# Optimization experiments

Hardware: AMD Instinct MI355X
Metric: run time of the kernel (lower is better)

The kernel has to match this reference:

```python
import jax, jax.numpy as jnp
import numpy as np

B, S, D, H = 2, 2048, 2048, 16
HD = D // H          # head_dim = 128
FF = 8192            # intermediate_size
LN_EPS = 1e-05
BIT_EPS = 1e-05


def _rope_tables(seq_len, head_dim):
    inv_freq = 1.0 / (10000.0 ** (np.arange(0, head_dim, 2, dtype=np.float64) / head_dim))
    ang = np.arange(seq_len, dtype=np.float64)[:, None] * inv_freq[None, :]  # [S, HD/2]
    ang = np.concatenate([ang, ang], axis=-1)  # [S, HD]
    return jnp.asarray(np.cos(ang), jnp.float32), jnp.asarray(np.sin(ang), jnp.float32)


def setup_inputs() -> dict:
    key = jax.random.key(0)
    ks = jax.random.split(key, 9)
    hidden_states = jax.random.normal(ks[0], (B, S, D), jnp.float32)
    # causal additive mask [1, S, S]
    causal = jnp.tril(jnp.ones((S, S), bool))
    attention_mask = jnp.where(causal, 0.0, -1e9)[None].astype(jnp.float32)
    cos, sin = _rope_tables(S, HD)
    w = lambda k, o, i: jax.random.normal(k, (o, i), jnp.float32) * 0.02
    return {
        'hidden_states': hidden_states,
        'attention_mask': attention_mask,
        'cos': cos, 'sin': sin,
        'wq': w(ks[1], D, D), 'wk': w(ks[2], D, D),
        'wv': w(ks[3], D, D), 'wo': w(ks[4], D, D),
        'wg': w(ks[5], FF, D), 'wu': w(ks[6], FF, D), 'wd': w(ks[7], D, FF),
        'ln1_w': jnp.ones((D,), jnp.float32),
        'ln2_w': jnp.ones((D,), jnp.float32),
    }


def bitlinear(x, w):
    # ternarize: clamp(round(w / (mean|w| + eps)), -1, 1); int8 cast in torch
    # breaks grad through the ternary values -> stop_gradient here.
    scale = jnp.mean(jnp.abs(w))
    tern = jax.lax.stop_gradient(jnp.clip(jnp.round(w / (scale + BIT_EPS)), -1.0, 1.0))
    # dequant = ternary * mean|w|, then standard linear (x @ W^T)
    return jnp.einsum('bsi,oi->bso', x, tern * scale)


def rmsnorm(x, w, eps=LN_EPS):
    var = jnp.mean(jnp.square(x.astype(jnp.float32)), axis=-1, keepdims=True)
    return w * (x * jax.lax.rsqrt(var + eps))


def rotate_half(x):
    x1, x2 = jnp.split(x, 2, axis=-1)
    return jnp.concatenate([-x2, x1], axis=-1)


def apply_rope(q, k, cos, sin):
    # q, k: [B, S, D] -> per-head rope -> back to [B, S, D]
    qh = q.reshape(B, S, H, HD)
    kh = k.reshape(B, S, H, HD)
    c = cos[None, :, None, :]
    s = sin[None, :, None, :]
    qe = qh * c + rotate_half(qh) * s
    ke = kh * c + rotate_half(kh) * s
    return qe.reshape(B, S, D), ke.reshape(B, S, D)


def reference(hidden_states, attention_mask, cos, sin,
              wq, wk, wv, wo, wg, wu, wd, ln1_w, ln2_w):
    residual = hidden_states
    # --- attention block ---
    x = rmsnorm(hidden_states, ln1_w)
    q = bitlinear(x, wq)
    k = bitlinear(x, wk)
    v = bitlinear(x, wv)
    q, k = apply_rope(q, k, cos, sin)
    # NOTE: scores over FULL hidden dim (no head split), scaled by sqrt(head_dim),
    # exactly as in the original module.
    scores = jnp.einsum('bsd,btd->bst', q, k) / jnp.sqrt(jnp.float32(HD))
    scores = scores + attention_mask
    probs = jax.nn.softmax(scores, axis=-1)
    attn_out = jnp.einsum('bst,btd->bsd', probs, v)
    attn_out = bitlinear(attn_out, wo)
    h = residual + attn_out
    # --- MLP block ---
    residual = h
    y = rmsnorm(h, ln2_w)
    gated = bitlinear(y, wg) * bitlinear(y, wu)
    out = bitlinear(gated, wd)
    return residual + out
```

## Files before the change

kernel.cpp:

```cpp
#include <hip/hip_runtime.h>
#include <stdint.h>

#define DEV __device__ __forceinline__

typedef __attribute__((ext_vector_type(8))) short short8;
typedef __attribute__((ext_vector_type(8))) __bf16 bf16x8;
typedef __attribute__((ext_vector_type(4))) float f32x4;

DEV unsigned short f2bf(float f) {
  union { float f; unsigned int u; } v; v.f = f;
  unsigned int r = v.u + 0x7fffu + ((v.u >> 16) & 1u);
  return (unsigned short)(r >> 16);
}
DEV float bf2f(unsigned short h) {
  union { unsigned int u; float f; } v; v.u = ((unsigned int)h) << 16;
  return v.f;
}
DEV f32x4 mfma16(short8 a, short8 b, f32x4 c) {
  return __builtin_amdgcn_mfma_f32_16x16x32_bf16(
      __builtin_bit_cast(bf16x8, a), __builtin_bit_cast(bf16x8, b), c, 0, 0, 0);
}
DEV void gload_lds16(const void* g, void* lds) {
  __builtin_amdgcn_global_load_lds(
      (const __attribute__((address_space(1))) void*)g,
      (__attribute__((address_space(3))) void*)lds, 16, 0, 0);
}

struct MArgs {
  const float* src[7];
  unsigned short* dst[7];
  int n[7];
  int sidx[7];
};

__global__ __launch_bounds__(256) void absmean_partial_multi(
    MArgs a, float* __restrict__ partial) {
  const int m = blockIdx.y;
  const float4* w4 = (const float4*)a.src[m];
  const int n4 = a.n[m] >> 2;
  float s = 0.f;
  for (int i = blockIdx.x * 256 + threadIdx.x; i < n4; i += 1024 * 256) {
    float4 v = w4[i];
    s += fabsf(v.x) + fabsf(v.y) + fabsf(v.z) + fabsf(v.w);
  }
#pragma unroll
  for (int mm = 1; mm < 64; mm <<= 1) s += __shfl_xor(s, mm);
  __shared__ float red[4];
  if ((threadIdx.x & 63) == 0) red[threadIdx.x >> 6] = s;
  __syncthreads();
  if (threadIdx.x == 0)
    partial[m * 1024 + blockIdx.x] = red[0] + red[1] + red[2] + red[3];
}

__global__ __launch_bounds__(256) void absmean_final(
    const float* __restrict__ partial, float* __restrict__ scales) {
  __shared__ double red[256];
  const int m = blockIdx.x;
  double s = 0.0;
  for (int i = threadIdx.x; i < 1024; i += 256) s += (double)partial[m * 1024 + i];
  red[threadIdx.x] = s;
  __syncthreads();
  for (int t = 128; t > 0; t >>= 1) {
    if (threadIdx.x < t) red[threadIdx.x] += red[threadIdx.x + t];
    __syncthreads();
  }
  if (threadIdx.x == 0) {
    const long long cnt = (m < 4) ? 4194304ll : 16777216ll;
    scales[m] = (float)(red[0] / (double)cnt);
  }
}

__global__ __launch_bounds__(256) void quantize_multi(
    MArgs a, const float* __restrict__ scales) {
  const int m = blockIdx.y;
  const float sc = scales[a.sidx[m]];
  const float inv = 1.f / (sc + 1e-5f);
  const float4* src = (const float4*)a.src[m];
  ushort4* dst = (ushort4*)a.dst[m];
  const int n4 = a.n[m] >> 2;
  for (int i = blockIdx.x * 256 + threadIdx.x; i < n4; i += 2048 * 256) {
    float4 v = src[i];
    ushort4 o;
    o.x = f2bf(fminf(fmaxf(rintf(v.x * inv), -1.f), 1.f) * sc);
    o.y = f2bf(fminf(fmaxf(rintf(v.y * inv), -1.f), 1.f) * sc);
    o.z = f2bf(fminf(fmaxf(rintf(v.z * inv), -1.f), 1.f) * sc);
    o.w = f2bf(fminf(fmaxf(rintf(v.w * inv), -1.f), 1.f) * sc);
    dst[i] = o;
  }
}

__global__ __launch_bounds__(256) void rmsnorm_k(
    const float* __restrict__ x, const float* __restrict__ wt,
    unsigned short* __restrict__ out) {
  const long long t = blockIdx.x;
  const float* xr = x + t * 2048;
  const int i0 = threadIdx.x * 8;
  float4 a = *(const float4*)(xr + i0);
  float4 b = *(const float4*)(xr + i0 + 4);
  float ss = a.x * a.x + a.y * a.y + a.z * a.z + a.w * a.w +
             b.x * b.x + b.y * b.y + b.z * b.z + b.w * b.w;
#pragma unroll
  for (int m = 1; m < 64; m <<= 1) ss += __shfl_xor(ss, m);
  __shared__ float red[4];
  if ((threadIdx.x & 63) == 0) red[threadIdx.x >> 6] = ss;
  __syncthreads();
  float tot = red[0] + red[1] + red[2] + red[3];
  float rs = rsqrtf(tot * (1.f / 2048.f) + 1e-5f);
  float4 wa = *(const float4*)(wt + i0);
  float4 wb = *(const float4*)(wt + i0 + 4);
  ushort4 o1, o2;
  o1.x = f2bf(a.x * wa.x * rs); o1.y = f2bf(a.y * wa.y * rs);
  o1.z = f2bf(a.z * wa.z * rs); o1.w = f2bf(a.w * wa.w * rs);
  o2.x = f2bf(b.x * wb.x * rs); o2.y = f2bf(b.y * wb.y * rs);
  o2.z = f2bf(b.z * wb.z * rs); o2.w = f2bf(b.w * wb.w * rs);
  *(ushort4*)(out + t * 2048 + i0) = o1;
  *(ushort4*)(out + t * 2048 + i0 + 4) = o2;
}

__global__ __launch_bounds__(256) void combine_rms(
    const float* __restrict__ ep, const float* __restrict__ p,
    const float* __restrict__ wt, float* __restrict__ hout,
    unsigned short* __restrict__ yout) {
  const long long t = blockIdx.x;
  const int i0 = threadIdx.x * 8;
  const long long base = t * 2048 + i0;
  float4 e1 = *(const float4*)(ep + base);
  float4 e2 = *(const float4*)(ep + base + 4);
  float4 p1 = *(const float4*)(p + base);
  float4 p2 = *(const float4*)(p + base + 4);
  float4 q1 = *(const float4*)(p + 8388608 + base);
  float4 q2 = *(const float4*)(p + 8388608 + base + 4);
  float h[8] = {e1.x + p1.x + q1.x, e1.y + p1.y + q1.y,
                e1.z + p1.z + q1.z, e1.w + p1.w + q1.w,
                e2.x + p2.x + q2.x, e2.y + p2.y + q2.y,
                e2.z + p2.z + q2.z, e2.w + p2.w + q2.w};
  float4 h1 = {h[0], h[1], h[2], h[3]};
  float4 h2 = {h[4], h[5], h[6], h[7]};
  *(float4*)(hout + base) = h1;
  *(float4*)(hout + base + 4) = h2;
  float ss = 0.f;
#pragma unroll
  for (int i = 0; i < 8; ++i) ss += h[i] * h[i];
#pragma unroll
  for (int m = 1; m < 64; m <<= 1) ss += __shfl_xor(ss, m);
  __shared__ float red[4];
  if ((threadIdx.x & 63) == 0) red[threadIdx.x >> 6] = ss;
  __syncthreads();
  const float tot = red[0] + red[1] + red[2] + red[3];
  const float rs = rsqrtf(tot * (1.f / 2048.f) + 1e-5f);
  float4 wa = *(const float4*)(wt + i0);
  float4 wb = *(const float4*)(wt + i0 + 4);
  ushort4 o1, o2;
  o1.x = f2bf(h[0] * wa.x * rs); o1.y = f2bf(h[1] * wa.y * rs);
  o1.z = f2bf(h[2] * wa.z * rs); o1.w = f2bf(h[3] * wa.w * rs);
  o2.x = f2bf(h[4] * wb.x * rs); o2.y = f2bf(h[5] * wb.y * rs);
  o2.z = f2bf(h[6] * wb.z * rs); o2.w = f2bf(h[7] * wb.w * rs);
  *(ushort4*)(yout + base) = o1;
  *(ushort4*)(yout + base + 4) = o2;
}

__global__ __launch_bounds__(256) void rope_k(
    const unsigned short* __restrict__ qkv, const float* __restrict__ cosT,
    const float* __restrict__ sinT, unsigned short* __restrict__ qr,
    unsigned short* __restrict__ kr, unsigned short* __restrict__ vt) {
  const long long gid = (long long)blockIdx.x * 256 + threadIdx.x;
  const int t = (int)(gid >> 10);
  const int r = (int)(gid & 1023);
  const int h = r >> 6, d = r & 63;
  const int s = t & 2047, b = t >> 11;
  const unsigned short* row = qkv + (long long)t * 6144;
  const float c = cosT[s * 128 + d], sn = sinT[s * 128 + d];
  const int col = h * 128 + d;
  const float SC = 0.08838834764831845f;
  float q1 = bf2f(row[col]), q2 = bf2f(row[col + 64]);
  float k1 = bf2f(row[2048 + col]), k2 = bf2f(row[2048 + col + 64]);
  long long ob = (long long)t * 2048 + col;
  qr[ob] = f2bf((q1 * c - q2 * sn) * SC);
  qr[ob + 64] = f2bf((q2 * c + q1 * sn) * SC);
  kr[ob] = f2bf(k1 * c - k2 * sn);
  kr[ob + 64] = f2bf(k2 * c + k1 * sn);
  vt[((long long)b * 2048 + col) * 2048 + s] = row[4096 + col];
  vt[((long long)b * 2048 + col + 64) * 2048 + s] = row[4096 + col + 64];
}

__global__ __launch_bounds__(256) void softmax_causal(
    const float* __restrict__ scores, unsigned short* __restrict__ probs) {
  const int r = blockIdx.x;
  const int s = r & 2047;
  const float* src = scores + (long long)r * 2048;
  unsigned short* dst = probs + (long long)r * 2048;
  const int L = s + 1;
  const int j0 = threadIdx.x * 8;
  float4 a = *(const float4*)(src + j0);
  float4 b = *(const float4*)(src + j0 + 4);
  float v[8] = {a.x, a.y, a.z, a.w, b.x, b.y, b.z, b.w};
  float mx = -1e30f;
#pragma unroll
  for (int i = 0; i < 8; ++i) {
    if (j0 + i >= L) v[i] = -1e30f;
    mx = fmaxf(mx, v[i]);
  }
#pragma unroll
  for (int m = 1; m < 64; m <<= 1) mx = fmaxf(mx, __shfl_xor(mx, m));
  __shared__ float redM[4], redS[4];
  if ((threadIdx.x & 63) == 0) redM[threadIdx.x >> 6] = mx;
  __syncthreads();
  mx = fmaxf(fmaxf(redM[0], redM[1]), fmaxf(redM[2], redM[3]));
  float sum = 0.f;
#pragma unroll
  for (int i = 0; i < 8; ++i) {
    v[i] = (j0 + i < L) ? __expf(v[i] - mx) : 0.f;
    sum += v[i];
  }
#pragma unroll
  for (int m = 1; m < 64; m <<= 1) sum += __shfl_xor(sum, m);
  if ((threadIdx.x & 63) == 0) redS[threadIdx.x >> 6] = sum;
  __syncthreads();
  const float inv = 1.f / (redS[0] + redS[1] + redS[2] + redS[3]);
  ushort4 o1, o2;
  o1.x = f2bf(v[0] * inv); o1.y = f2bf(v[1] * inv);
  o1.z = f2bf(v[2] * inv); o1.w = f2bf(v[3] * inv);
  o2.x = f2bf(v[4] * inv); o2.y = f2bf(v[5] * inv);
  o2.z = f2bf(v[6] * inv); o2.w = f2bf(v[7] * inv);
  *(ushort4*)(dst + j0) = o1;
  *(ushort4*)(dst + j0 + 4) = o2;
}

template <int EPI, int CAUSAL>
__global__ __launch_bounds__(512, 2) void gemm256(
    const unsigned short* __restrict__ A, const unsigned short* __restrict__ Bw,
    void* __restrict__ Cp, const void* __restrict__ Ep,
    int N, int K, int nbx, int kLen, int ngTot,
    long long sAz, long long sBz, long long zCout) {
  __shared__ __align__(16) unsigned short lds[4 * 2 * 8192];
  __shared__ __align__(16) unsigned short ldsDummy[512];
  const int tid = threadIdx.x;
  const int wid = tid >> 6, l = tid & 63;
  const int wr = wid >> 2, wcn = wid & 3;

  const int nwg = gridDim.x;
  const int q8 = nwg >> 3;
  const int lin = (blockIdx.x & 7) * q8 + (blockIdx.x >> 3);
  const int t32 = lin >> 5, r32 = lin & 31;
  const int tpr = nbx >> 3;
  const int tm = t32 / tpr, tn = t32 - tm * tpr;
  const long long m0 = (long long)(tm * 4 + (r32 >> 3)) * 256;
  const long long n0 = (long long)(tn * 8 + (r32 & 7)) * 256;
  if (CAUSAL == 1 && n0 > m0) return;
  const int z = blockIdx.z;
  A += z * sAz;
  Bw += z * sBz;
  const long long kbase = (long long)z * kLen;
  const long long zofs = (long long)z * zCout;
  int ng = ngTot;
  if (CAUSAL == 2) {
    const int lim = (int)((m0 + 256) >> 5);
    ng = lim < ng ? lim : ng;
  }

  const int stRow = (l >> 2);
  const int stCol = (((l & 3) ^ ((l >> 3) & 3))) * 8;
  auto stage = [&](int chunk, int sslot) {
    if (chunk < ng) {
      char* base = (char*)lds + (sslot * 2) * 16384;
      const long long kcol = kbase + (long long)chunk * 32 + stCol;
#pragma unroll
      for (int i = 0; i < 2; ++i) {
        const int row = (wid * 2 + i) * 16 + stRow;
        gload_lds16(&A[(m0 + row) * K + kcol], base + (wid * 2 + i) * 1024);
        gload_lds16(&Bw[(n0 + row) * K + kcol],
                    base + 16384 + (wid * 2 + i) * 1024);
      }
    } else {
#pragma unroll
      for (int i = 0; i < 4; ++i) gload_lds16(&A[m0 * K], (char*)ldsDummy);
    }
  };

  const int ar = l & 15;
  const int rj = ((l >> 4) ^ ((l >> 1) & 3)) << 4;
  const int aoff = (wr * 128 + ar) * 64 + rj;
  const int boff = (wcn * 64 + ar) * 64 + rj;

  f32x4 acc[8][4] = {};
  short8 aX[4], bX[4], aY[4], bY[4];

  stage(0, 0); stage(1, 1); stage(2, 2);
  asm volatile("s_waitcnt vmcnt(4)" ::: "memory");
  __builtin_amdgcn_s_barrier();
#pragma unroll
  for (int m = 0; m < 4; ++m)
    aX[m] = *(const short8*)((const char*)lds + aoff + m * 1024);
#pragma unroll
  for (int n = 0; n < 4; ++n)
    bX[n] = *(const short8*)((const char*)lds + 16384 + boff + n * 1024);

#define CHUNK_BODY(SLOT, NSLOT, SYNC, cur03, curB, nxt03, nxtB, cc)            \
  {                                                                            \
    const char* sAc = (const char*)lds + (SLOT * 2) * 16384;                   \
    const char* sAn = (const char*)lds + (NSLOT * 2) * 16384;                  \
    const char* sBn = (const char*)lds + (NSLOT * 2 + 1) * 16384;              \
    short8 a47[4];                                                             \
    _Pragma("unroll") for (int m = 0; m < 4; ++m)                              \
        a47[m] = *(const short8*)(sAc + aoff + 4096 + m * 1024);               \
    stage((cc) + 3, (SLOT + 3) & 3);                                           \
    __builtin_amdgcn_s_setprio(1);                                             \
    _Pragma("unroll") for (int m = 0; m < 4; ++m)                              \
      _Pragma("unroll") for (int n = 0; n < 4; ++n)                            \
          acc[m][n] = mfma16(cur03[m], curB[n], acc[m][n]);                    \
    __builtin_amdgcn_s_setprio(0);                                             \
    if (SYNC) {                                                                \
      asm volatile("s_waitcnt vmcnt(4)" ::: "memory");                         \
      __builtin_amdgcn_s_barrier();                                            \
    }                                                                          \
    _Pragma("unroll") for (int m = 0; m < 4; ++m)                              \
        nxt03[m] = *(const short8*)(sAn + aoff + m * 1024);                    \
    _Pragma("unroll") for (int n = 0; n < 4; ++n)                              \
        nxtB[n] = *(const short8*)(sBn + boff + n * 1024);                     \
    __builtin_amdgcn_s_setprio(1);                                             \
    _Pragma("unroll") for (int m = 0; m < 4; ++m)                              \
      _Pragma("unroll") for (int n = 0; n < 4; ++n)                            \
          acc[m + 4][n] = mfma16(a47[m], curB[n], acc[m + 4][n]);              \
    __builtin_amdgcn_s_setprio(0);                                             \
  }

  for (int c = 0; c < ng; c += 4) {
    CHUNK_BODY(0, 1, false, aX, bX, aY, bY, c);
    CHUNK_BODY(1, 2, true, aY, bY, aX, bX, c + 1);
    CHUNK_BODY(2, 3, false, aX, bX, aY, bY, c + 2);
    CHUNK_BODY(3, 0, true, aY, bY, aX, bX, c + 3);
  }
#undef CHUNK_BODY
  asm volatile("s_waitcnt vmcnt(0)" ::: "memory");
  __builtin_amdgcn_s_barrier();

  const int orow = (l >> 4) * 4, ocol = l & 15;
#pragma unroll
  for (int m = 0; m < 8; ++m)
#pragma unroll
    for (int n = 0; n < 4; ++n)
#pragma unroll
      for (int r = 0; r < 4; ++r) {
        const long long gr = m0 + wr * 128 + m * 16 + orow + r;
        const long long gc = n0 + wcn * 64 + n * 16 + ocol;
        const long long idx = zofs + gr * N + gc;
        const float v = acc[m][n][r];
        if (EPI == 0) {
          ((unsigned short*)Cp)[idx] = f2bf(v);
        } else if (EPI == 2) {
          ((unsigned short*)Cp)[idx] = f2bf(bf2f(((const unsigned short*)Ep)[idx]) * v);
        } else {
          ((float*)Cp)[idx] = v;
        }
      }
}

__global__ __launch_bounds__(256) void combine2(
    const float* __restrict__ ep, const float* __restrict__ p,
    float* __restrict__ out, long long n4) {
  const float4* e4 = (const float4*)ep;
  const float4* p4 = (const float4*)p;
  float4* o4 = (float4*)out;
  for (long long i = blockIdx.x * 256 + threadIdx.x; i < n4; i += 2048 * 256) {
    float4 a = e4[i], b = p4[i], c = p4[i + n4];
    float4 o;
    o.x = a.x + b.x + c.x; o.y = a.y + b.y + c.y;
    o.z = a.z + b.z + c.z; o.w = a.w + b.w + c.w;
    o4[i] = o;
  }
}

extern "C" void kernel_launch(void* const* d_in, const int* in_sizes, int n_in,
                              void* d_out, int out_size, void* d_ws, size_t ws_size,
                              hipStream_t stream) {
  (void)in_sizes; (void)n_in; (void)out_size; (void)ws_size;
  const float* hidden = (const float*)d_in[0];
  const float* cosT = (const float*)d_in[2];
  const float* sinT = (const float*)d_in[3];
  const float* wq = (const float*)d_in[4];
  const float* wk = (const float*)d_in[5];
  const float* wv = (const float*)d_in[6];
  const float* wo = (const float*)d_in[7];
  const float* wg = (const float*)d_in[8];
  const float* wu = (const float*)d_in[9];
  const float* wd = (const float*)d_in[10];
  const float* ln1 = (const float*)d_in[11];
  const float* ln2 = (const float*)d_in[12];

  const size_t MB = 1ull << 20;
  char* ws = (char*)d_ws;
  unsigned short* xn    = (unsigned short*)(ws + 0);
  unsigned short* wqkvq = (unsigned short*)(ws + 16 * MB);
  unsigned short* qkv   = (unsigned short*)(ws + 40 * MB);
  unsigned short* qrb   = (unsigned short*)(ws + 88 * MB);
  unsigned short* krb   = (unsigned short*)(ws + 104 * MB);
  unsigned short* vtb   = (unsigned short*)(ws + 120 * MB);
  float*          scoresB = (float*)(ws + 0);
  unsigned short* probsB  = (unsigned short*)(ws + 40 * MB);
  float*          part   = (float*)(ws + 0);
  unsigned short* wgq   = (unsigned short*)(ws + 0);
  unsigned short* wuq   = (unsigned short*)(ws + 32 * MB);
  unsigned short* gbuf  = (unsigned short*)(ws + 64 * MB);
  unsigned short* attnb = (unsigned short*)(ws + 136 * MB);
  unsigned short* woq   = (unsigned short*)(ws + 152 * MB);
  float*          hbuf  = (float*)(ws + 160 * MB);
  unsigned short* ybuf  = (unsigned short*)(ws + 192 * MB);
  unsigned short* gated = (unsigned short*)(ws + 208 * MB);
  unsigned short* wdq   = (unsigned short*)(ws + 272 * MB);
  float* wspart         = (float*)(ws + 304 * MB);
  float* scales         = (float*)(ws + 304 * MB + 32768);

  MArgs am;
  am.src[0] = wq; am.src[1] = wk; am.src[2] = wv; am.src[3] = wo;
  am.src[4] = wg; am.src[5] = wu; am.src[6] = wd;
  am.n[0] = am.n[1] = am.n[2] = am.n[3] = 4194304;
  am.n[4] = am.n[5] = am.n[6] = 16777216;
  for (int i = 0; i < 7; ++i) { am.dst[i] = nullptr; am.sidx[i] = i; }
  absmean_partial_multi<<<dim3(1024, 7), 256, 0, stream>>>(am, wspart);
  absmean_final<<<7, 256, 0, stream>>>(wspart, scales);

  MArgs qe;
  qe.src[0] = wq; qe.dst[0] = wqkvq;            qe.n[0] = 4194304;  qe.sidx[0] = 0;
  qe.src[1] = wk; qe.dst[1] = wqkvq + 4194304;  qe.n[1] = 4194304;  qe.sidx[1] = 1;
  qe.src[2] = wv; qe.dst[2] = wqkvq + 8388608;  qe.n[2] = 4194304;  qe.sidx[2] = 2;
  qe.src[3] = wo; qe.dst[3] = woq;              qe.n[3] = 4194304;  qe.sidx[3] = 3;
  qe.src[4] = wd; qe.dst[4] = wdq;              qe.n[4] = 16777216; qe.sidx[4] = 6;
  qe.src[5] = wq; qe.dst[5] = nullptr; qe.n[5] = 0; qe.sidx[5] = 0;
  qe.src[6] = wq; qe.dst[6] = nullptr; qe.n[6] = 0; qe.sidx[6] = 0;
  quantize_multi<<<dim3(2048, 5), 256, 0, stream>>>(qe, scales);

  rmsnorm_k<<<4096, 256, 0, stream>>>(hidden, ln1, xn);

  gemm256<0, 0><<<dim3(384, 1, 1), 512, 0, stream>>>(
      xn, wqkvq, qkv, nullptr, 6144, 2048, 24, 2048, 64, 0, 0, 0);

  rope_k<<<16384, 256, 0, stream>>>(qkv, cosT, sinT, qrb, krb, vtb);

  gemm256<4, 1><<<dim3(64, 1, 2), 512, 0, stream>>>(
      qrb, krb, scoresB, nullptr, 2048, 2048, 8, 0, 64, 4194304, 4194304, 4194304);
  softmax_causal<<<4096, 256, 0, stream>>>(scoresB, probsB);
  gemm256<0, 2><<<dim3(64, 1, 2), 512, 0, stream>>>(
      probsB, vtb, attnb, nullptr, 2048, 2048, 8, 0, 64, 4194304, 4194304, 4194304);

  gemm256<4, 0><<<dim3(128, 1, 2), 512, 0, stream>>>(
      attnb, woq, part, nullptr, 2048, 2048, 8, 1024, 32, 0, 0, 8388608);
  combine_rms<<<4096, 256, 0, stream>>>(hidden, part, ln2, hbuf, ybuf);

  MArgs ql;
  ql.src[0] = wg; ql.dst[0] = wgq; ql.n[0] = 16777216; ql.sidx[0] = 4;
  ql.src[1] = wu; ql.dst[1] = wuq; ql.n[1] = 16777216; ql.sidx[1] = 5;
  for (int i = 2; i < 7; ++i) { ql.src[i] = wg; ql.dst[i] = nullptr; ql.n[i] = 0; ql.sidx[i] = 0; }
  quantize_multi<<<dim3(2048, 2), 256, 0, stream>>>(ql, scales);

  gemm256<0, 0><<<dim3(512, 1, 1), 512, 0, stream>>>(
      ybuf, wgq, gbuf, nullptr, 8192, 2048, 32, 2048, 64, 0, 0, 0);
  gemm256<2, 0><<<dim3(512, 1, 1), 512, 0, stream>>>(
      ybuf, wuq, gated, gbuf, 8192, 2048, 32, 2048, 64, 0, 0, 0);

  gemm256<4, 0><<<dim3(128, 1, 2), 512, 0, stream>>>(
      gated, wdq, part, nullptr, 2048, 8192, 8, 4096, 128, 0, 0, 8388608);
  combine2<<<2048, 256, 0, stream>>>(hbuf, part, (float*)d_out, 2097152);
}
```

Baseline: 818.8 us.

## Use 128x128 attention GEMMs, tiled V transpose, and bf16 split-K partials

```diff
diff --git a/kernel.cpp b/kernel.cpp
--- a/kernel.cpp
+++ b/kernel.cpp
@@ -118,7 +118,7 @@
 }
 
 __global__ __launch_bounds__(256) void combine_rms(
-    const float* __restrict__ ep, const float* __restrict__ p,
+    const float* __restrict__ ep, const unsigned short* __restrict__ p,
     const float* __restrict__ wt, float* __restrict__ hout,
     unsigned short* __restrict__ yout) {
   const long long t = blockIdx.x;
@@ -126,14 +126,13 @@
   const long long base = t * 2048 + i0;
   float4 e1 = *(const float4*)(ep + base);
   float4 e2 = *(const float4*)(ep + base + 4);
-  float4 p1 = *(const float4*)(p + base);
-  float4 p2 = *(const float4*)(p + base + 4);
-  float4 q1 = *(const float4*)(p + 8388608 + base);
-  float4 q2 = *(const float4*)(p + 8388608 + base + 4);
-  float h[8] = {e1.x + p1.x + q1.x, e1.y + p1.y + q1.y,
-                e1.z + p1.z + q1.z, e1.w + p1.w + q1.w,
-                e2.x + p2.x + q2.x, e2.y + p2.y + q2.y,
-                e2.z + p2.z + q2.z, e2.w + p2.w + q2.w};
+  short8 pa = *(const short8*)(p + base);
+  short8 pb = *(const short8*)(p + 8388608 + base);
+  const float e[8] = {e1.x, e1.y, e1.z, e1.w, e2.x, e2.y, e2.z, e2.w};
+  float h[8];
+#pragma unroll
+  for (int i = 0; i < 8; ++i)
+    h[i] = e[i] + bf2f((unsigned short)pa[i]) + bf2f((unsigned short)pb[i]);
   float4 h1 = {h[0], h[1], h[2], h[3]};
   float4 h2 = {h[4], h[5], h[6], h[7]};
   *(float4*)(hout + base) = h1;
@@ -159,15 +158,36 @@
   *(ushort4*)(yout + base + 4) = o2;
 }
 
+__global__ __launch_bounds__(256) void combine2(
+    const float* __restrict__ ep, const unsigned short* __restrict__ p,
+    float* __restrict__ out) {
+  const long long base = (long long)blockIdx.x * 2048 + threadIdx.x * 8;
+  float4 e1 = *(const float4*)(ep + base);
+  float4 e2 = *(const float4*)(ep + base + 4);
+  short8 pa = *(const short8*)(p + base);
+  short8 pb = *(const short8*)(p + 8388608 + base);
+  float4 o1, o2;
+  o1.x = e1.x + bf2f((unsigned short)pa[0]) + bf2f((unsigned short)pb[0]);
+  o1.y = e1.y + bf2f((unsigned short)pa[1]) + bf2f((unsigned short)pb[1]);
+  o1.z = e1.z + bf2f((unsigned short)pa[2]) + bf2f((unsigned short)pb[2]);
+  o1.w = e1.w + bf2f((unsigned short)pa[3]) + bf2f((unsigned short)pb[3]);
+  o2.x = e2.x + bf2f((unsigned short)pa[4]) + bf2f((unsigned short)pb[4]);
+  o2.y = e2.y + bf2f((unsigned short)pa[5]) + bf2f((unsigned short)pb[5]);
+  o2.z = e2.z + bf2f((unsigned short)pa[6]) + bf2f((unsigned short)pb[6]);
+  o2.w = e2.w + bf2f((unsigned short)pa[7]) + bf2f((unsigned short)pb[7]);
+  *(float4*)(out + base) = o1;
+  *(float4*)(out + base + 4) = o2;
+}
+
 __global__ __launch_bounds__(256) void rope_k(
     const unsigned short* __restrict__ qkv, const float* __restrict__ cosT,
     const float* __restrict__ sinT, unsigned short* __restrict__ qr,
-    unsigned short* __restrict__ kr, unsigned short* __restrict__ vt) {
+    unsigned short* __restrict__ kr) {
   const long long gid = (long long)blockIdx.x * 256 + threadIdx.x;
   const int t = (int)(gid >> 10);
   const int r = (int)(gid & 1023);
   const int h = r >> 6, d = r & 63;
-  const int s = t & 2047, b = t >> 11;
+  const int s = t & 2047;
   const unsigned short* row = qkv + (long long)t * 6144;
   const float c = cosT[s * 128 + d], sn = sinT[s * 128 + d];
   const int col = h * 128 + d;
@@ -179,8 +199,30 @@
   qr[ob + 64] = f2bf((q2 * c + q1 * sn) * SC);
   kr[ob] = f2bf(k1 * c - k2 * sn);
   kr[ob + 64] = f2bf(k2 * c + k1 * sn);
-  vt[((long long)b * 2048 + col) * 2048 + s] = row[4096 + col];
-  vt[((long long)b * 2048 + col + 64) * 2048 + s] = row[4096 + col + 64];
+}
+
+__global__ __launch_bounds__(256) void vtrans_k(
+    const unsigned short* __restrict__ qkv, unsigned short* __restrict__ vt) {
+  __shared__ unsigned short tile[64][66];
+  const int tt = blockIdx.x << 6, dd = blockIdx.y << 6;
+  const long long b = blockIdx.z;
+  const int r0 = threadIdx.x >> 4, c0 = (threadIdx.x & 15) << 2;
+#pragma unroll
+  for (int i = 0; i < 4; ++i) {
+    const int row = r0 + i * 16;
+    ushort4 v = *(const ushort4*)&qkv[(b * 2048 + tt + row) * 6144 + 4096 + dd + c0];
+    tile[row][c0] = v.x; tile[row][c0 + 1] = v.y;
+    tile[row][c0 + 2] = v.z; tile[row][c0 + 3] = v.w;
+  }
+  __syncthreads();
+#pragma unroll
+  for (int i = 0; i < 4; ++i) {
+    const int d = r0 + i * 16;
+    ushort4 o;
+    o.x = tile[c0][d]; o.y = tile[c0 + 1][d];
+    o.z = tile[c0 + 2][d]; o.w = tile[c0 + 3][d];
+    *(ushort4*)&vt[(b * 2048 + dd + d) * 2048 + tt + c0] = o;
+  }
 }
 
 __global__ __launch_bounds__(256) void softmax_causal(
@@ -224,6 +266,77 @@
   o2.z = f2bf(v[6] * inv); o2.w = f2bf(v[7] * inv);
   *(ushort4*)(dst + j0) = o1;
   *(ushort4*)(dst + j0 + 4) = o2;
+}
+
+template <int EPI, int CAUSAL>
+__global__ __launch_bounds__(256) void gemm_nt(
+    const unsigned short* __restrict__ A, const unsigned short* __restrict__ Bw,
+    void* __restrict__ Cp, int M, int N, int K,
+    long long sAz, long long sBz, long long sCz) {
+  const long long m0 = (long long)blockIdx.y * 128;
+  const long long n0 = (long long)blockIdx.x * 128;
+  if (CAUSAL == 1 && n0 > m0 + 127) return;
+  __shared__ __align__(16) unsigned short sA[2][128 * 32];
+  __shared__ __align__(16) unsigned short sB[2][128 * 32];
+  const int tid = threadIdx.x;
+  const int w = tid >> 6, l = tid & 63;
+  const long long z = blockIdx.z;
+  A += z * sAz;
+  Bw += z * sBz;
+  const long long cofs = z * sCz;
+  const int wr = w >> 1, wc = w & 1;
+  const int lrow = l & 15, lk = (l >> 4) * 8;
+
+  f32x4 acc[4][4] = {};
+  int nk = K >> 5;
+  if (CAUSAL == 2) nk = (int)((m0 + 128) >> 5);
+  int cur = 0;
+
+  auto stage = [&](int buf, int k0) {
+#pragma unroll
+    for (int i = 0; i < 2; ++i) {
+      const int flat = (w * 2 + i) * 64 + l;
+      const int row = flat >> 2;
+      const int col = (flat & 3) * 8;
+      gload_lds16(&A[(m0 + row) * K + k0 + col], (char*)&sA[buf][0] + (w * 2 + i) * 1024);
+      gload_lds16(&Bw[(n0 + row) * K + k0 + col], (char*)&sB[buf][0] + (w * 2 + i) * 1024);
+    }
+  };
+
+  stage(0, 0);
+  __syncthreads();
+  for (int kt = 0; kt < nk; ++kt) {
+    if (kt + 1 < nk) stage(cur ^ 1, (kt + 1) << 5);
+    short8 af[4], bfr[4];
+#pragma unroll
+    for (int m = 0; m < 4; ++m)
+      af[m] = *(const short8*)&sA[cur][(wr * 64 + m * 16 + lrow) * 32 + lk];
+#pragma unroll
+    for (int n = 0; n < 4; ++n)
+      bfr[n] = *(const short8*)&sB[cur][(wc * 64 + n * 16 + lrow) * 32 + lk];
+#pragma unroll
+    for (int m = 0; m < 4; ++m)
+#pragma unroll
+      for (int n = 0; n < 4; ++n)
+        acc[m][n] = mfma16(af[m], bfr[n], acc[m][n]);
+    __syncthreads();
+    cur ^= 1;
+  }
+
+  const int orow = (l >> 4) * 4, ocol = l & 15;
+#pragma unroll
+  for (int m = 0; m < 4; ++m)
+#pragma unroll
+    for (int n = 0; n < 4; ++n)
+#pragma unroll
+      for (int r = 0; r < 4; ++r) {
+        long long gr = m0 + wr * 64 + m * 16 + orow + r;
+        long long gc = n0 + wc * 64 + n * 16 + ocol;
+        long long idx = cofs + gr * N + gc;
+        float v = acc[m][n][r];
+        if (EPI == 0) ((unsigned short*)Cp)[idx] = f2bf(v);
+        else ((float*)Cp)[idx] = v;
+      }
 }
 
 template <int EPI, int CAUSAL>
@@ -355,21 +468,6 @@
       }
 }
 
-__global__ __launch_bounds__(256) void combine2(
-    const float* __restrict__ ep, const float* __restrict__ p,
-    float* __restrict__ out, long long n4) {
-  const float4* e4 = (const float4*)ep;
-  const float4* p4 = (const float4*)p;
-  float4* o4 = (float4*)out;
-  for (long long i = blockIdx.x * 256 + threadIdx.x; i < n4; i += 2048 * 256) {
-    float4 a = e4[i], b = p4[i], c = p4[i + n4];
-    float4 o;
-    o.x = a.x + b.x + c.x; o.y = a.y + b.y + c.y;
-    o.z = a.z + b.z + c.z; o.w = a.w + b.w + c.w;
-    o4[i] = o;
-  }
-}
-
 extern "C" void kernel_launch(void* const* d_in, const int* in_sizes, int n_in,
                               void* d_out, int out_size, void* d_ws, size_t ws_size,
                               hipStream_t stream) {
@@ -397,7 +495,7 @@
   unsigned short* vtb   = (unsigned short*)(ws + 120 * MB);
   float*          scoresB = (float*)(ws + 0);
   unsigned short* probsB  = (unsigned short*)(ws + 40 * MB);
-  float*          part   = (float*)(ws + 0);
+  unsigned short* partb = (unsigned short*)(ws + 0);
   unsigned short* wgq   = (unsigned short*)(ws + 0);
   unsigned short* wuq   = (unsigned short*)(ws + 32 * MB);
   unsigned short* gbuf  = (unsigned short*)(ws + 64 * MB);
@@ -434,17 +532,18 @@
   gemm256<0, 0><<<dim3(384, 1, 1), 512, 0, stream>>>(
       xn, wqkvq, qkv, nullptr, 6144, 2048, 24, 2048, 64, 0, 0, 0);
 
-  rope_k<<<16384, 256, 0, stream>>>(qkv, cosT, sinT, qrb, krb, vtb);
-
-  gemm256<4, 1><<<dim3(64, 1, 2), 512, 0, stream>>>(
-      qrb, krb, scoresB, nullptr, 2048, 2048, 8, 0, 64, 4194304, 4194304, 4194304);
+  rope_k<<<16384, 256, 0, stream>>>(qkv, cosT, sinT, qrb, krb);
+  vtrans_k<<<dim3(32, 32, 2), 256, 0, stream>>>(qkv, vtb);
+
+  gemm_nt<4, 1><<<dim3(16, 16, 2), 256, 0, stream>>>(
+      qrb, krb, scoresB, 2048, 2048, 2048, 4194304, 4194304, 4194304);
   softmax_causal<<<4096, 256, 0, stream>>>(scoresB, probsB);
-  gemm256<0, 2><<<dim3(64, 1, 2), 512, 0, stream>>>(
-      probsB, vtb, attnb, nullptr, 2048, 2048, 8, 0, 64, 4194304, 4194304, 4194304);
-
-  gemm256<4, 0><<<dim3(128, 1, 2), 512, 0, stream>>>(
-      attnb, woq, part, nullptr, 2048, 2048, 8, 1024, 32, 0, 0, 8388608);
-  combine_rms<<<4096, 256, 0, stream>>>(hidden, part, ln2, hbuf, ybuf);
+  gemm_nt<0, 2><<<dim3(16, 16, 2), 256, 0, stream>>>(
+      probsB, vtb, attnb, 2048, 2048, 2048, 4194304, 4194304, 4194304);
+
+  gemm256<0, 0><<<dim3(128, 1, 2), 512, 0, stream>>>(
+      attnb, woq, partb, nullptr, 2048, 2048, 8, 1024, 32, 0, 0, 8388608);
+  combine_rms<<<4096, 256, 0, stream>>>(hidden, partb, ln2, hbuf, ybuf);
 
   MArgs ql;
   ql.src[0] = wg; ql.dst[0] = wgq; ql.n[0] = 16777216; ql.sidx[0] = 4;
@@ -457,7 +556,7 @@
   gemm256<2, 0><<<dim3(512, 1, 1), 512, 0, stream>>>(
       ybuf, wuq, gated, gbuf, 8192, 2048, 32, 2048, 64, 0, 0, 0);
 
-  gemm256<4, 0><<<dim3(128, 1, 2), 512, 0, stream>>>(
-      gated, wdq, part, nullptr, 2048, 8192, 8, 4096, 128, 0, 0, 8388608);
-  combine2<<<2048, 256, 0, stream>>>(hbuf, part, (float*)d_out, 2097152);
-}
+  gemm256<0, 0><<<dim3(128, 1, 2), 512, 0, stream>>>(
+      gated, wdq, partb, nullptr, 2048, 8192, 8, 4096, 128, 0, 0, 8388608);
+  combine2<<<4096, 256, 0, stream>>>(hbuf, partb, (float*)d_out);
+}
```

Measured after the change: 772.5 us. 5.7% less time.
